# Kernel optimization log

Measured on AMD Instinct MI355X. Metric: run time of the kernel, lower is better.

The kernel has to match this reference:

```python
import jax, jax.numpy as jnp
import numpy as np

N, F_IN, UNITS, HEADS = 4096, 128, 64, 4
EDGE_P = 0.01  # adjacency density


def setup_inputs() -> dict:
    key = jax.random.key(0)
    k1, k2, k3, k4, k5 = jax.random.split(key, 5)
    inputs = jax.random.normal(k1, (N, F_IN), dtype=jnp.float32)
    adj = jax.random.bernoulli(k2, EDGE_P, (N, N)).astype(jnp.float32)
    # glorot-normal-ish parameter scales
    w = jax.random.normal(k3, (F_IN, UNITS), dtype=jnp.float32) * np.float32(np.sqrt(2.0 / (F_IN + UNITS)))
    attn_w1 = jax.random.normal(k4, (UNITS, HEADS), dtype=jnp.float32) * np.float32(np.sqrt(2.0 / (UNITS + HEADS)))
    attn_w2 = jax.random.normal(k5, (UNITS, HEADS), dtype=jnp.float32) * np.float32(np.sqrt(2.0 / (UNITS + HEADS)))
    return {"inputs": inputs, "adj": adj, "w": w, "attn_w1": attn_w1, "attn_w2": attn_w2}


def reference(inputs, adj, w, attn_w1, attn_w2):
    # dropout=0, bias=0, final_layer=False, activation=relu
    x = inputs @ w                                  # [N, U]
    e1 = x @ attn_w1                                # [N, H]
    e2 = x @ attn_w2                                # [N, H]
    # coeffs[i, j, h] = relu(e1[i, h] + e2[j, h])
    coeffs = jax.nn.relu(e1[:, None, :] + e2[None, :, :])   # [N, N, H]
    # NOTE: original multiplies by adj (zeros -> logit 0, not -inf) then softmax over j
    scores = adj[:, :, None] * coeffs               # [N, N, H]
    attn = jax.nn.softmax(scores, axis=1)           # normalize over neighbors j
    # per-head aggregation, concat heads -> [N, H*U] (head-major blocks)
    out = jnp.einsum("ijh,ju->ihu", attn, x).reshape(N, HEADS * UNITS)
    return jax.nn.relu(out)
```

## Files before the change

kernel.cpp:

```cpp
#include <hip/hip_runtime.h>
#include <hip/hip_bf16.h>

#define N_NODES 4096
#define F_IN    128
#define UNITS   64
#define HEADS   4
#define WT_PITCH 132
#define CHUNK   128

__global__ __launch_bounds__(256) void k1(const float* __restrict__ inputs,
                                          const float* __restrict__ w,
                                          const float* __restrict__ aw1,
                                          const float* __restrict__ aw2,
                                          float* __restrict__ x,
                                          float* __restrict__ e1,
                                          float* __restrict__ e2,
                                          float* __restrict__ partial) {
    __shared__ float w_t[UNITS * WT_PITCH];
    __shared__ float in_lds[16 * F_IN];
    __shared__ float x_lds[16 * 65];

    const int t = threadIdx.x;
    const int b = blockIdx.x;
    const int row0 = b * 16;

    for (int idx = t; idx < F_IN * UNITS; idx += 256) {
        const int u = idx & 63;
        const int k = idx >> 6;
        w_t[u * WT_PITCH + k] = w[idx];
    }
    {
        const float4* src = (const float4*)(inputs + (size_t)row0 * F_IN);
        float4* dst = (float4*)in_lds;
        for (int idx = t; idx < 16 * F_IN / 4; idx += 256) dst[idx] = src[idx];
    }
    __syncthreads();

    const int u = t & 63;
    const int rg = t >> 6;
    float acc0 = 0.f, acc1 = 0.f, acc2 = 0.f, acc3 = 0.f;
    const float4* wrow = (const float4*)(w_t + u * WT_PITCH);
    const float4* i0 = (const float4*)(in_lds + (rg * 4 + 0) * F_IN);
    const float4* i1 = (const float4*)(in_lds + (rg * 4 + 1) * F_IN);
    const float4* i2 = (const float4*)(in_lds + (rg * 4 + 2) * F_IN);
    const float4* i3 = (const float4*)(in_lds + (rg * 4 + 3) * F_IN);
#pragma unroll 8
    for (int c = 0; c < F_IN / 4; c++) {
        const float4 wv = wrow[c];
        float4 v;
        v = i0[c]; acc0 = fmaf(wv.x, v.x, fmaf(wv.y, v.y, fmaf(wv.z, v.z, fmaf(wv.w, v.w, acc0))));
        v = i1[c]; acc1 = fmaf(wv.x, v.x, fmaf(wv.y, v.y, fmaf(wv.z, v.z, fmaf(wv.w, v.w, acc1))));
        v = i2[c]; acc2 = fmaf(wv.x, v.x, fmaf(wv.y, v.y, fmaf(wv.z, v.z, fmaf(wv.w, v.w, acc2))));
        v = i3[c]; acc3 = fmaf(wv.x, v.x, fmaf(wv.y, v.y, fmaf(wv.z, v.z, fmaf(wv.w, v.w, acc3))));
    }
    x_lds[(rg * 4 + 0) * 65 + u] = acc0;
    x_lds[(rg * 4 + 1) * 65 + u] = acc1;
    x_lds[(rg * 4 + 2) * 65 + u] = acc2;
    x_lds[(rg * 4 + 3) * 65 + u] = acc3;
    x[(size_t)(row0 + rg * 4 + 0) * UNITS + u] = acc0;
    x[(size_t)(row0 + rg * 4 + 1) * UNITS + u] = acc1;
    x[(size_t)(row0 + rg * 4 + 2) * UNITS + u] = acc2;
    x[(size_t)(row0 + rg * 4 + 3) * UNITS + u] = acc3;
    __syncthreads();

    if (t < 128) {
        const int r = t >> 3;
        const int rem = t & 7;
        const int h = rem & 3;
        const bool first = rem < 4;
        const float* aw = first ? aw1 : aw2;
        float s = 0.f;
#pragma unroll 8
        for (int uu = 0; uu < UNITS; uu++)
            s += x_lds[r * 65 + uu] * aw[uu * HEADS + h];
        (first ? e1 : e2)[(size_t)(row0 + r) * HEADS + h] = s;
    }

    if (t < 64) {
        float s = 0.f;
#pragma unroll
        for (int r = 0; r < 16; r++) s += x_lds[r * 65 + t];
        partial[b * 64 + t] = s;
    }
}

__global__ __launch_bounds__(256) void k1b(const float* __restrict__ partial,
                                           float* __restrict__ S) {
    __shared__ float red[4][64];
    const int u = threadIdx.x & 63;
    const int q = threadIdx.x >> 6;
    float s = 0.f;
#pragma unroll 8
    for (int b = q; b < 256; b += 4) s += partial[b * 64 + u];
    red[q][u] = s;
    __syncthreads();
    if (threadIdx.x < 64) S[u] = red[0][u] + red[1][u] + red[2][u] + red[3][u];
}

__global__ __launch_bounds__(256) void k2(const float* __restrict__ adj,
                                          const float* __restrict__ x,
                                          const float* __restrict__ e1,
                                          const float* __restrict__ e2,
                                          const float* __restrict__ S,
                                          float* __restrict__ out) {
    __shared__ unsigned short nbr[N_NODES];
    __shared__ float wgt[CHUNK * 4];
    __shared__ int cnt;

    const int i = blockIdx.x;
    const int t = threadIdx.x;

    if (t == 0) cnt = 0;
    __syncthreads();

    const float4* arow = (const float4*)(adj + (size_t)i * N_NODES);
#pragma unroll
    for (int it = 0; it < 4; it++) {
        const int c = t + it * 256;
        const float4 v = arow[c];
        const int base = c * 4;
        if (v.x != 0.f) nbr[atomicAdd(&cnt, 1)] = (unsigned short)(base + 0);
        if (v.y != 0.f) nbr[atomicAdd(&cnt, 1)] = (unsigned short)(base + 1);
        if (v.z != 0.f) nbr[atomicAdd(&cnt, 1)] = (unsigned short)(base + 2);
        if (v.w != 0.f) nbr[atomicAdd(&cnt, 1)] = (unsigned short)(base + 3);
    }
    __syncthreads();

    const int n = cnt;
    const int h = t >> 6;
    const int u = t & 63;

    const float4 e1v = *(const float4*)(e1 + (size_t)i * HEADS);

    float acc = 0.f;
    float den = 0.f;

    for (int base = 0; base < n; base += CHUNK) {
        const int m = min(n - base, CHUNK);

        if (t < m) {
            const int j = nbr[base + t];
            const float4 e2v = *(const float4*)(e2 + (size_t)j * HEADS);
            float4 wv;
            wv.x = __expf(fmaxf(e1v.x + e2v.x, 0.f)) - 1.f;
            wv.y = __expf(fmaxf(e1v.y + e2v.y, 0.f)) - 1.f;
            wv.z = __expf(fmaxf(e1v.z + e2v.z, 0.f)) - 1.f;
            wv.w = __expf(fmaxf(e1v.w + e2v.w, 0.f)) - 1.f;
            *(float4*)(wgt + t * 4) = wv;
        }
        __syncthreads();

#pragma unroll 4
        for (int k = 0; k < m; k++) {
            const int j = nbr[base + k];
            const float wv = wgt[k * 4 + h];
            den += wv;
            acc = fmaf(wv, x[j * UNITS + u], acc);
        }
        __syncthreads();
    }

    const float numer = S[u] + acc;
    const float denom = (float)N_NODES + den;
    out[(size_t)i * (HEADS * UNITS) + t] = fmaxf(numer / denom, 0.f);
}

extern "C" void kernel_launch(void* const* d_in, const int* in_sizes, int n_in,
                              void* d_out, int out_size, void* d_ws, size_t ws_size,
                              hipStream_t stream) {
    const float* inputs = (const float*)d_in[0];
    const float* adj    = (const float*)d_in[1];
    const float* w      = (const float*)d_in[2];
    const float* aw1    = (const float*)d_in[3];
    const float* aw2    = (const float*)d_in[4];
    float* out = (float*)d_out;

    float* ws = (float*)d_ws;
    float* x       = ws;
    float* e1      = ws + 262144;
    float* e2      = ws + 262144 + 16384;
    float* partial = ws + 262144 + 2 * 16384;
    float* S       = ws + 262144 + 3 * 16384;

    k1<<<256, 256, 0, stream>>>(inputs, w, aw1, aw2, x, e1, e2, partial);
    k1b<<<1, 256, 0, stream>>>(partial, S);
    k2<<<N_NODES, 256, 0, stream>>>(adj, x, e1, e2, S, out);
}
```

Baseline: 121.1 us.

## Stage neighbor x rows in LDS and hoist adjacency loads in aggregation kernel

The aggregation kernel now cooperatively gathers each chunk of neighbor x rows into shared memory once, instead of having each of the four head groups read them from global memory separately. The inner loop then reads only from LDS, and the chunk size is halved to bound LDS use. It also issues all four adjacency float4 loads before the compaction atomics, and caches the attention weights in LDS in the first kernel. The added staging pass and LDS footprint (16KB more per block) may reduce occupancy and add an extra barrier-bound phase per chunk.

```diff
diff --git a/kernel.cpp b/kernel.cpp
--- a/kernel.cpp
+++ b/kernel.cpp
@@ -6,7 +6,7 @@
 #define UNITS   64
 #define HEADS   4
 #define WT_PITCH 132
-#define CHUNK   128
+#define CHUNK   64
 
 __global__ __launch_bounds__(256) void k1(const float* __restrict__ inputs,
                                           const float* __restrict__ w,
@@ -19,6 +19,7 @@
     __shared__ float w_t[UNITS * WT_PITCH];
     __shared__ float in_lds[16 * F_IN];
     __shared__ float x_lds[16 * 65];
+    __shared__ float aw_lds[2 * UNITS * HEADS];
 
     const int t = threadIdx.x;
     const int b = blockIdx.x;
@@ -33,6 +34,10 @@
         const float4* src = (const float4*)(inputs + (size_t)row0 * F_IN);
         float4* dst = (float4*)in_lds;
         for (int idx = t; idx < 16 * F_IN / 4; idx += 256) dst[idx] = src[idx];
+    }
+    if (t < UNITS * HEADS) {
+        aw_lds[t] = aw1[t];
+        aw_lds[UNITS * HEADS + t] = aw2[t];
     }
     __syncthreads();
 
@@ -68,7 +73,7 @@
         const int rem = t & 7;
         const int h = rem & 3;
         const bool first = rem < 4;
-        const float* aw = first ? aw1 : aw2;
+        const float* aw = aw_lds + (first ? 0 : UNITS * HEADS);
         float s = 0.f;
 #pragma unroll 8
         for (int uu = 0; uu < UNITS; uu++)
@@ -104,6 +109,7 @@
                                           const float* __restrict__ S,
                                           float* __restrict__ out) {
     __shared__ unsigned short nbr[N_NODES];
+    __shared__ float xs[CHUNK * UNITS];
     __shared__ float wgt[CHUNK * 4];
     __shared__ int cnt;
 
@@ -114,15 +120,31 @@
     __syncthreads();
 
     const float4* arow = (const float4*)(adj + (size_t)i * N_NODES);
-#pragma unroll
-    for (int it = 0; it < 4; it++) {
-        const int c = t + it * 256;
-        const float4 v = arow[c];
-        const int base = c * 4;
-        if (v.x != 0.f) nbr[atomicAdd(&cnt, 1)] = (unsigned short)(base + 0);
-        if (v.y != 0.f) nbr[atomicAdd(&cnt, 1)] = (unsigned short)(base + 1);
-        if (v.z != 0.f) nbr[atomicAdd(&cnt, 1)] = (unsigned short)(base + 2);
-        if (v.w != 0.f) nbr[atomicAdd(&cnt, 1)] = (unsigned short)(base + 3);
+    const float4 v0 = arow[t];
+    const float4 v1 = arow[t + 256];
+    const float4 v2 = arow[t + 512];
+    const float4 v3 = arow[t + 768];
+    {
+        const int b0 = t * 4;
+        if (v0.x != 0.f) nbr[atomicAdd(&cnt, 1)] = (unsigned short)(b0 + 0);
+        if (v0.y != 0.f) nbr[atomicAdd(&cnt, 1)] = (unsigned short)(b0 + 1);
+        if (v0.z != 0.f) nbr[atomicAdd(&cnt, 1)] = (unsigned short)(b0 + 2);
+        if (v0.w != 0.f) nbr[atomicAdd(&cnt, 1)] = (unsigned short)(b0 + 3);
+        const int b1 = (t + 256) * 4;
+        if (v1.x != 0.f) nbr[atomicAdd(&cnt, 1)] = (unsigned short)(b1 + 0);
+        if (v1.y != 0.f) nbr[atomicAdd(&cnt, 1)] = (unsigned short)(b1 + 1);
+        if (v1.z != 0.f) nbr[atomicAdd(&cnt, 1)] = (unsigned short)(b1 + 2);
+        if (v1.w != 0.f) nbr[atomicAdd(&cnt, 1)] = (unsigned short)(b1 + 3);
+        const int b2 = (t + 512) * 4;
+        if (v2.x != 0.f) nbr[atomicAdd(&cnt, 1)] = (unsigned short)(b2 + 0);
+        if (v2.y != 0.f) nbr[atomicAdd(&cnt, 1)] = (unsigned short)(b2 + 1);
+        if (v2.z != 0.f) nbr[atomicAdd(&cnt, 1)] = (unsigned short)(b2 + 2);
+        if (v2.w != 0.f) nbr[atomicAdd(&cnt, 1)] = (unsigned short)(b2 + 3);
+        const int b3 = (t + 768) * 4;
+        if (v3.x != 0.f) nbr[atomicAdd(&cnt, 1)] = (unsigned short)(b3 + 0);
+        if (v3.y != 0.f) nbr[atomicAdd(&cnt, 1)] = (unsigned short)(b3 + 1);
+        if (v3.z != 0.f) nbr[atomicAdd(&cnt, 1)] = (unsigned short)(b3 + 2);
+        if (v3.w != 0.f) nbr[atomicAdd(&cnt, 1)] = (unsigned short)(b3 + 3);
     }
     __syncthreads();
 
@@ -148,14 +170,18 @@
             wv.w = __expf(fmaxf(e1v.w + e2v.w, 0.f)) - 1.f;
             *(float4*)(wgt + t * 4) = wv;
         }
+        for (int idx = t; idx < m * UNITS; idx += 256) {
+            const int k = idx >> 6;
+            const int uu = idx & 63;
+            xs[idx] = x[(size_t)nbr[base + k] * UNITS + uu];
+        }
         __syncthreads();
 
-#pragma unroll 4
+#pragma unroll 8
         for (int k = 0; k < m; k++) {
-            const int j = nbr[base + k];
             const float wv = wgt[k * 4 + h];
             den += wv;
-            acc = fmaf(wv, x[j * UNITS + u], acc);
+            acc = fmaf(wv, xs[k * UNITS + u], acc);
         }
         __syncthreads();
     }
```

Result: no change. 119.2 us (-1.6%).
